# Performance work log

Measured on AMD Instinct MI355X. Metric: run time of the kernel, lower is better.

Reference implementation:

```python
import jax, jax.numpy as jnp
import numpy as np

EPS = 1e-5

def conv1x1(x, W, b):
    # x: (B,C,N,K), W: (O,C), b: (O,)
    return jnp.einsum('oc,bcnk->bonk', W, x) + b[None, :, None, None]

def group_norm(x, G, w, b):
    B, C, N, K = x.shape
    xg = x.reshape(B, G, C // G, N, K)
    mu = xg.mean(axis=(2, 3, 4), keepdims=True)
    var = xg.var(axis=(2, 3, 4), keepdims=True)
    xn = ((xg - mu) / jnp.sqrt(var + EPS)).reshape(B, C, N, K)
    return xn * w[None, :, None, None] + b[None, :, None, None]

def setup_inputs() -> dict:
    key = jax.random.key(0)
    ks = jax.random.split(key, 20)
    B, N, K = 4, 4096, 32
    C_in1, C_in2, C1, C2, C_out = 128, 128, 64, 64, 128
    Ccat = C1 + C2          # 128
    inter_C = min(Ccat, C_out)  # 128
    s = 0.05
    return {
        'feat': jax.random.normal(ks[0], (B, C_in1, N), jnp.float32),
        'grouped_feat': jax.random.normal(ks[1], (B, C_in2, N, K), jnp.float32),
        'grouped_feat_out': jax.random.normal(ks[2], (B, C_out, N, K), jnp.float32),
        'count': jax.random.randint(ks[3], (B, N), 0, K, jnp.int32),
        'W_feat': jax.random.normal(ks[4], (C1, C_in1), jnp.float32) * s,
        'b_feat': jax.random.normal(ks[5], (C1,), jnp.float32) * s,
        'W_grp': jax.random.normal(ks[6], (C2, C_in2), jnp.float32) * s,
        'b_grp': jax.random.normal(ks[7], (C2,), jnp.float32) * s,
        'gn1_w': jnp.ones((Ccat,), jnp.float32),
        'gn1_b': jnp.zeros((Ccat,), jnp.float32),
        'W_wc1': jax.random.normal(ks[8], (inter_C, Ccat), jnp.float32) * s,
        'b_wc1': jax.random.normal(ks[9], (inter_C,), jnp.float32) * s,
        'gn2_w': jnp.ones((inter_C,), jnp.float32),
        'gn2_b': jnp.zeros((inter_C,), jnp.float32),
        'W_wc2': jax.random.normal(ks[10], (C_out, inter_C), jnp.float32) * s,
        'b_wc2': jax.random.normal(ks[11], (C_out,), jnp.float32) * s,
        'W_fo': jax.random.normal(ks[12], (C_out, C_out), jnp.float32) * s,
        'b_fo': jax.random.normal(ks[13], (C_out,), jnp.float32) * s,
        'gn3_w': jnp.ones((C_out,), jnp.float32),
        'gn3_b': jnp.zeros((C_out,), jnp.float32),
    }

def reference(feat, grouped_feat, grouped_feat_out, count,
              W_feat, b_feat, W_grp, b_grp,
              gn1_w, gn1_b, W_wc1, b_wc1, gn2_w, gn2_b, W_wc2, b_wc2,
              W_fo, b_fo, gn3_w, gn3_b):
    K = grouped_feat.shape[-1]
    G = 32
    # feat_conv on feat.unsqueeze(-1), then expand along K
    feat1 = jnp.einsum('oc,bcn->bon', W_feat, feat) + b_feat[None, :, None]
    feat1 = jnp.broadcast_to(feat1[..., None], feat1.shape + (K,))
    g1 = conv1x1(grouped_feat, W_grp, b_grp)
    total = jnp.concatenate([feat1, g1], axis=1)  # (B, C1+C2, N, K)
    # weight_conv: ReLU -> GN -> conv -> ReLU -> GN -> conv
    x = jax.nn.relu(total)
    x = group_norm(x, G, gn1_w, gn1_b)
    x = conv1x1(x, W_wc1, b_wc1)
    x = jax.nn.relu(x)
    x = group_norm(x, G, gn2_w, gn2_b)
    scores = conv1x1(x, W_wc2, b_wc2)  # (B, C_out, N, K)
    # count-based mask over K, count clamped to >= 1
    cnt = jnp.clip(count, 1, None)
    mask = (jnp.arange(K)[None, None, :] < cnt[:, :, None]).astype(scores.dtype)  # (B,N,K)
    mask = mask[:, None, :, :]
    scores = scores * mask + (-1e9) * (1.0 - mask)
    weight = jax.nn.softmax(scores, axis=-1)
    # feat_out_conv: conv -> GN -> ReLU
    gfo = conv1x1(grouped_feat_out, W_fo, b_fo)
    gfo = jax.nn.relu(group_norm(gfo, G, gn3_w, gn3_b))
    return (gfo * weight).sum(axis=-1)  # (B, C_out, N)
```

## Files before the change

### kernel.cpp

```cpp
#include <hip/hip_runtime.h>


#define B_   4
#define N_   4096
#define KK_  32
#define NK_  131072
#define C_   128
#define EPSV 1e-5f

typedef _Float16 hf8 __attribute__((ext_vector_type(8)));
typedef _Float16 hf4 __attribute__((ext_vector_type(4)));
typedef float    f4  __attribute__((ext_vector_type(4)));

__global__ void prep_k(const float* __restrict__ Wgrp, const float* __restrict__ Wfo,
                       _Float16* __restrict__ Wgrp_h, _Float16* __restrict__ Wfo_h,
                       float* __restrict__ stats)
{
    int tid = blockIdx.x * 256 + threadIdx.x;
    if (tid < 64 * 128)  Wgrp_h[tid] = (_Float16)Wgrp[tid];
    if (tid < 128 * 128) Wfo_h[tid]  = (_Float16)Wfo[tid];
    if (tid < 768)       stats[tid]  = 0.0f;
}

__global__ void feat_k(const float* __restrict__ feat, const float* __restrict__ Wf,
                       const float* __restrict__ bfeat, float* __restrict__ f1r,
                       float* __restrict__ stats1)
{
    __shared__ float fs[128][64];
    __shared__ float gst[32];
    int tid = threadIdx.x, b = blockIdx.y, n0 = blockIdx.x * 64;
    if (tid < 32) gst[tid] = 0.0f;
    for (int i = tid; i < 128 * 64; i += 256) {
        int ci = i >> 6, n = i & 63;
        fs[ci][n] = feat[((size_t)b * 128 + ci) * N_ + n0 + n];
    }
    __syncthreads();
    int n = tid & 63, cb = (tid >> 6) * 16;
    float gs1[4] = {0,0,0,0}, gs2[4] = {0,0,0,0};
    for (int j = 0; j < 16; j++) {
        int c = cb + j;
        float a = bfeat[c];
        #pragma unroll 16
        for (int ci = 0; ci < 128; ci++) a += Wf[c * 128 + ci] * fs[ci][n];
        a = fmaxf(a, 0.0f);
        f1r[((size_t)b * 64 + c) * N_ + n0 + n] = a;
        gs1[j >> 2] += a; gs2[j >> 2] += a * a;
    }
    for (int g = 0; g < 4; g++) {
        atomicAdd(&gst[((cb >> 2) + g) * 2 + 0], gs1[g]);
        atomicAdd(&gst[((cb >> 2) + g) * 2 + 1], gs2[g]);
    }
    __syncthreads();
    if (tid < 32) atomicAdd(&stats1[b * 64 + tid], gst[tid]);
}

__global__ void fold_k(const float* __restrict__ stats, const float* __restrict__ gw,
                       const float* __restrict__ gb, const float* __restrict__ Wsrc,
                       const float* __restrict__ bsrc, _Float16* __restrict__ Wdst,
                       float* __restrict__ bdst, float* __restrict__ sdst,
                       float* __restrict__ tdst, int lowcnt)
{
    int b = blockIdx.x, tid = threadIdx.x;
    __shared__ float ss[128], st[128];
    if (tid < 128) {
        int c = tid, g = c >> 2;
        float d  = (lowcnt && g < 16) ? (4.0f * N_) : (4.0f * NK_);
        float S1 = stats[(b * 32 + g) * 2], S2 = stats[(b * 32 + g) * 2 + 1];
        float mu = S1 / d;
        float var = fmaxf(S2 / d - mu * mu, 0.0f);
        float s = gw[c] * rsqrtf(var + EPSV);
        float t = gb[c] - mu * s;
        ss[c] = s; st[c] = t;
        if (sdst) { sdst[b * 128 + c] = s; tdst[b * 128 + c] = t; }
    }
    __syncthreads();
    if (Wdst && tid < 128) {
        int co = tid;
        float a = bsrc[co];
        for (int c = 0; c < 128; c++) {
            float w = Wsrc[co * 128 + c];
            a += w * st[c];
            Wdst[((size_t)b * 128 + co) * 128 + c] = (_Float16)(w * ss[c]);
        }
        bdst[b * 128 + co] = a;
    }
}

__global__ void upass_k(const float* __restrict__ f1r, const _Float16* __restrict__ W1p,
                        const float* __restrict__ b1p, float* __restrict__ u)
{
    int b = blockIdx.y, n0 = blockIdx.x * 32, tid = threadIdx.x;
    __shared__ float fs[64][33];
    __shared__ _Float16 wl[128][68];
    for (int i = tid; i < 64 * 32; i += 256) {
        int c = i >> 5, n = i & 31;
        fs[c][n] = f1r[((size_t)b * 64 + c) * N_ + n0 + n];
    }
    for (int i = tid; i < 128 * 64; i += 256) {
        int co = i >> 6, c = i & 63;
        wl[co][c] = W1p[((size_t)b * 128 + co) * 128 + c];
    }
    __syncthreads();
    int co = tid & 127, nh = tid >> 7;
    float bb = b1p[b * 128 + co];
    for (int ps = 0; ps < 16; ps++) {
        int n = nh * 16 + ps;
        float a = bb;
        #pragma unroll 16
        for (int c = 0; c < 64; c++) a += (float)wl[co][c] * fs[c][n];
        u[((size_t)b * N_ + n0 + n) * C_ + co] = a;
    }
}

template<int CIN, int COUT, int TP, bool SRCF32, int EPI, bool HASU,
         int WRS, int WCOFF, int COOFF, bool WPB, bool BPB>
__global__ void __launch_bounds__(256, 2) gemm_k(
    const void* srcv, const _Float16* __restrict__ W, const float* __restrict__ bias,
    _Float16* out, float* __restrict__ stats, const float* __restrict__ u,
    const int* __restrict__ cnt)
{
    constexpr int KC  = CIN / 32;
    constexpr int WCO = (COUT == 128) ? 2 : 1;
    constexpr int WP  = 4 / WCO;
    constexpr int TILES = NK_ / TP;
    constexpr int NGR = TP / 32;

    __shared__ _Float16 xs[TP][CIN + 8];
    __shared__ float bstat[(EPI != 2) ? COUT * 2 : 1];
    __shared__ float uld[HASU ? NGR * COUT : 1];
    __shared__ int   cld[(EPI == 2) ? NGR : 1];

    const int tid  = threadIdx.x;
    const int lane = tid & 63;
    const int wave = tid >> 6;
    const int l15  = lane & 15;
    const int q    = lane >> 4;
    const int wm   = wave % WP;
    const int wn   = wave / WP;
    const int b    = blockIdx.y;

    hf8 bf[4][KC];
    const _Float16* Wb = W + (WPB ? (size_t)b * COUT * WRS : 0);
    #pragma unroll
    for (int nt = 0; nt < 4; nt++) {
        int co = wn * 64 + nt * 16 + l15;
        #pragma unroll
        for (int kc = 0; kc < KC; kc++)
            bf[nt][kc] = *(const hf8*)(Wb + (size_t)co * WRS + WCOFF + kc * 32 + q * 8);
    }
    float biasr[4];
    #pragma unroll
    for (int nt = 0; nt < 4; nt++) {
        int co = wn * 64 + nt * 16 + l15;
        biasr[nt] = bias ? bias[(BPB ? b * COUT : 0) + co] : 0.0f;
    }
    if (EPI != 2) for (int i = tid; i < COUT * 2; i += 256) bstat[i] = 0.0f;

    constexpr int TPG = TP / 4;
    constexpr int CQP = 256 / TPG;
    constexpr int PASSES = CIN / (4 * CQP);
    const int tp = tid % TPG;
    const int cq = tid / TPG;

    for (int t = blockIdx.x; t < TILES; t += gridDim.x) {
        const int pbase = t * TP;
        #pragma unroll
        for (int ps = 0; ps < PASSES; ps++) {
            int c0 = (ps * CQP + cq) * 4;
            _Float16 hv[4][4];
            if (SRCF32) {
                const float* s = (const float*)srcv;
                #pragma unroll
                for (int r = 0; r < 4; r++) {
                    f4 v = *(const f4*)(s + ((size_t)(b * CIN + c0 + r)) * NK_ + pbase + tp * 4);
                    #pragma unroll
                    for (int i = 0; i < 4; i++) hv[r][i] = (_Float16)v[i];
                }
            } else {
                const _Float16* s = (const _Float16*)srcv;
                #pragma unroll
                for (int r = 0; r < 4; r++) {
                    hf4 v = *(const hf4*)(s + ((size_t)(b * CIN + c0 + r)) * NK_ + pbase + tp * 4);
                    #pragma unroll
                    for (int i = 0; i < 4; i++) hv[r][i] = v[i];
                }
            }
            #pragma unroll
            for (int i = 0; i < 4; i++) {
                hf4 w = { hv[0][i], hv[1][i], hv[2][i], hv[3][i] };
                *(hf4*)&xs[tp * 4 + i][c0] = w;
            }
        }
        if (HASU)
            for (int i = tid; i < NGR * COUT; i += 256) {
                int ni = i / COUT, co = i % COUT;
                uld[ni * COUT + co] = u[((size_t)b * N_ + (pbase >> 5) + ni) * C_ + co];
            }
        if (EPI == 2 && tid < NGR) {
            int c = cnt[b * N_ + (pbase >> 5) + tid];
            cld[tid] = c < 1 ? 1 : c;
        }
        __syncthreads();

        f4 acc[4][4];
        #pragma unroll
        for (int mt = 0; mt < 4; mt++)
            #pragma unroll
            for (int nt = 0; nt < 4; nt++) {
                float v;
                if (HASU) v = uld[(wm * 2 + (mt >> 1)) * COUT + wn * 64 + nt * 16 + l15];
                else      v = biasr[nt];
                acc[mt][nt] = f4{v, v, v, v};
            }

        #pragma unroll
        for (int kc = 0; kc < KC; kc++) {
            hf8 af[4];
            #pragma unroll
            for (int mt = 0; mt < 4; mt++)
                af[mt] = *(const hf8*)&xs[wm * 64 + mt * 16 + l15][kc * 32 + q * 8];
            #pragma unroll
            for (int mt = 0; mt < 4; mt++)
                #pragma unroll
                for (int nt = 0; nt < 4; nt++)
                    acc[mt][nt] = __builtin_amdgcn_mfma_f32_16x16x32_f16(
                        af[mt], bf[nt][kc], acc[mt][nt], 0, 0, 0);
        }

        if constexpr (EPI != 2) {
            #pragma unroll
            for (int nt = 0; nt < 4; nt++) {
                int co = wn * 64 + nt * 16 + l15;
                float s1 = 0.0f, s2 = 0.0f;
                #pragma unroll
                for (int mt = 0; mt < 4; mt++) {
                    f4 a = acc[mt][nt];
                    #pragma unroll
                    for (int i = 0; i < 4; i++) {
                        if (EPI == 0) a[i] = fmaxf(a[i], 0.0f);
                        s1 += a[i]; s2 += a[i] * a[i];
                    }
                    hf4 hv = { (_Float16)a[0], (_Float16)a[1], (_Float16)a[2], (_Float16)a[3] };
                    *(hf4*)(out + ((size_t)(b * COUT + co)) * NK_ + pbase + wm * 64 + mt * 16 + q * 4) = hv;
                }
                s1 += __shfl_xor(s1, 16); s1 += __shfl_xor(s1, 32);
                s2 += __shfl_xor(s2, 16); s2 += __shfl_xor(s2, 32);
                if (q == 0) {
                    atomicAdd(&bstat[co * 2 + 0], s1);
                    atomicAdd(&bstat[co * 2 + 1], s2);
                }
            }
        } else {
            #pragma unroll
            for (int nt = 0; nt < 4; nt++) {
                float mx0 = -3e38f, mx1 = -3e38f;
                #pragma unroll
                for (int mt = 0; mt < 4; mt++) {
                    int cv = cld[wm * 2 + (mt >> 1)];
                    #pragma unroll
                    for (int r = 0; r < 4; r++) {
                        int k = (mt & 1) * 16 + q * 4 + r;
                        float v = acc[mt][nt][r];
                        if (k >= cv) v = -1e9f;
                        acc[mt][nt][r] = v;
                        if (mt < 2) mx0 = fmaxf(mx0, v); else mx1 = fmaxf(mx1, v);
                    }
                }
                mx0 = fmaxf(mx0, __shfl_xor(mx0, 16)); mx0 = fmaxf(mx0, __shfl_xor(mx0, 32));
                mx1 = fmaxf(mx1, __shfl_xor(mx1, 16)); mx1 = fmaxf(mx1, __shfl_xor(mx1, 32));
                float sm0 = 0.0f, sm1 = 0.0f;
                #pragma unroll
                for (int mt = 0; mt < 4; mt++) {
                    float m = (mt < 2) ? mx0 : mx1;
                    #pragma unroll
                    for (int r = 0; r < 4; r++) {
                        float e = __expf(acc[mt][nt][r] - m);
                        acc[mt][nt][r] = e;
                        if (mt < 2) sm0 += e; else sm1 += e;
                    }
                }
                sm0 += __shfl_xor(sm0, 16); sm0 += __shfl_xor(sm0, 32);
                sm1 += __shfl_xor(sm1, 16); sm1 += __shfl_xor(sm1, 32);
                float i0 = 1.0f / sm0, i1 = 1.0f / sm1;
                int co = wn * 64 + nt * 16 + l15;
                #pragma unroll
                for (int mt = 0; mt < 4; mt++) {
                    float inv = (mt < 2) ? i0 : i1;
                    hf4 hv = { (_Float16)(acc[mt][nt][0] * inv), (_Float16)(acc[mt][nt][1] * inv),
                               (_Float16)(acc[mt][nt][2] * inv), (_Float16)(acc[mt][nt][3] * inv) };
                    *(hf4*)(out + ((size_t)(b * COUT + co)) * NK_ + pbase + wm * 64 + mt * 16 + q * 4) = hv;
                }
            }
        }
        __syncthreads();
    }

    if (EPI != 2 && stats) {
        for (int i = tid; i < COUT * 2; i += 256) {
            int co = i >> 1, j = i & 1;
            int g = (co + COOFF) >> 2;
            atomicAdd(&stats[(b * 32 + g) * 2 + j], bstat[i]);
        }
    }
}

__global__ void final_k(const _Float16* __restrict__ y3, const _Float16* __restrict__ wgt,
                        const float* __restrict__ s3, const float* __restrict__ t3,
                        float* __restrict__ outp)
{
    int idx = blockIdx.x * 256 + threadIdx.x;
    int bc = idx >> 12;
    float sc = s3[bc], tc = t3[bc];
    const _Float16* yp = y3 + (size_t)idx * 32;
    const _Float16* wp = wgt + (size_t)idx * 32;
    float accv = 0.0f;
    #pragma unroll
    for (int i = 0; i < 4; i++) {
        hf8 yv = *(const hf8*)(yp + i * 8);
        hf8 wv = *(const hf8*)(wp + i * 8);
        #pragma unroll
        for (int j = 0; j < 8; j++) {
            float g = fmaxf(sc * (float)yv[j] + tc, 0.0f);
            accv += g * (float)wv[j];
        }
    }
    outp[idx] = accv;
}

extern "C" void kernel_launch(void* const* d_in, const int* in_sizes, int n_in,
                              void* d_out, int out_size, void* d_ws, size_t ws_size,
                              hipStream_t stream)
{
    (void)in_sizes; (void)n_in; (void)out_size; (void)ws_size;
    const float* feat   = (const float*)d_in[0];
    const float* gf     = (const float*)d_in[1];
    const float* gfo    = (const float*)d_in[2];
    const int*   count  = (const int*)d_in[3];
    const float* W_feat = (const float*)d_in[4];
    const float* b_feat = (const float*)d_in[5];
    const float* W_grp  = (const float*)d_in[6];
    const float* b_grp  = (const float*)d_in[7];
    const float* gn1w   = (const float*)d_in[8];
    const float* gn1b   = (const float*)d_in[9];
    const float* W_wc1  = (const float*)d_in[10];
    const float* b_wc1  = (const float*)d_in[11];
    const float* gn2w   = (const float*)d_in[12];
    const float* gn2b   = (const float*)d_in[13];
    const float* W_wc2  = (const float*)d_in[14];
    const float* b_wc2  = (const float*)d_in[15];
    const float* W_fo   = (const float*)d_in[16];
    const float* b_fo   = (const float*)d_in[17];
    const float* gn3w   = (const float*)d_in[18];
    const float* gn3b   = (const float*)d_in[19];
    float* out = (float*)d_out;

    char* ws = (char*)d_ws;
    size_t o = 0;
    auto alloc = [&](size_t bytes) { size_t r = o; o += (bytes + 255) & ~(size_t)255; return r; };
    _Float16* x1h    = (_Float16*)(ws + alloc((size_t)64 * B_ * NK_ * 2));
    _Float16* x2     = (_Float16*)(ws + alloc((size_t)128 * B_ * NK_ * 2));
    _Float16* y3     = (_Float16*)(ws + alloc((size_t)128 * B_ * NK_ * 2));
    float*    f1r    = (float*)(ws + alloc((size_t)B_ * 64 * N_ * 4));
    float*    u      = (float*)(ws + alloc((size_t)B_ * N_ * 128 * 4));
    float*    stats1 = (float*)(ws + alloc(256 * 4));
    float*    stats2 = (float*)(ws + alloc(256 * 4));
    float*    stats3 = (float*)(ws + alloc(256 * 4));
    _Float16* Wgrp_h = (_Float16*)(ws + alloc(64 * 128 * 2));
    _Float16* Wfo_h  = (_Float16*)(ws + alloc(128 * 128 * 2));
    _Float16* W1p    = (_Float16*)(ws + alloc((size_t)B_ * 128 * 128 * 2));
    float*    b1p    = (float*)(ws + alloc(B_ * 128 * 4));
    _Float16* W2p    = (_Float16*)(ws + alloc((size_t)B_ * 128 * 128 * 2));
    float*    b2p    = (float*)(ws + alloc(B_ * 128 * 4));
    float*    s3     = (float*)(ws + alloc(B_ * 128 * 4));
    float*    t3     = (float*)(ws + alloc(B_ * 128 * 4));
    _Float16* wgt    = x2;

    prep_k<<<64, 256, 0, stream>>>(W_grp, W_fo, Wgrp_h, Wfo_h, stats1);
    feat_k<<<dim3(64, B_), 256, 0, stream>>>(feat, W_feat, b_feat, f1r, stats1);
    gemm_k<128, 64, 256, true, 0, false, 128, 0, 64, false, false>
        <<<dim3(128, B_), 256, 0, stream>>>(gf, Wgrp_h, b_grp, x1h, stats1, nullptr, nullptr);
    fold_k<<<B_, 256, 0, stream>>>(stats1, gn1w, gn1b, W_wc1, b_wc1, W1p, b1p, nullptr, nullptr, 1);
    upass_k<<<dim3(128, B_), 256, 0, stream>>>(f1r, W1p, b1p, u);
    gemm_k<64, 128, 128, false, 0, true, 128, 64, 0, true, false>
        <<<dim3(256, B_), 256, 0, stream>>>(x1h, W1p, nullptr, x2, stats2, u, nullptr);
    gemm_k<128, 128, 128, true, 1, false, 128, 0, 0, false, false>
        <<<dim3(256, B_), 256, 0, stream>>>(gfo, Wfo_h, b_fo, y3, stats3, nullptr, nullptr);
    fold_k<<<B_, 256, 0, stream>>>(stats2, gn2w, gn2b, W_wc2, b_wc2, W2p, b2p, nullptr, nullptr, 0);
    fold_k<<<B_, 256, 0, stream>>>(stats3, gn3w, gn3b, nullptr, nullptr, nullptr, nullptr, s3, t3, 0);
    gemm_k<128, 128, 128, false, 2, false, 128, 0, 0, true, true>
        <<<dim3(256, B_), 256, 0, stream>>>(x2, W2p, b2p, wgt, nullptr, nullptr, count);
    final_k<<<(B_ * 128 * N_) / 256, 256, 0, stream>>>(y3, wgt, s3, t3, out);
}
```

Before: 1.226 ms.

## Prefetch next tile's inputs into registers to overlap with MFMA compute

Software-pipelines the persistent GEMM loop: the next tile's source activations, u-vectors and counts are loaded into registers while the current tile computes, and are written to LDS at the start of the following iteration. Full __syncthreads are replaced with raw s_barrier plus lgkmcnt waits, so the vmcnt drain is skipped and global loads can stay in flight across the barrier. This adds register pressure under launch_bounds(256,2), which may cause spills or lower occupancy, and the hand-placed barriers bring some risk of LDS races.

```diff
diff --git a/kernel.cpp b/kernel.cpp
--- a/kernel.cpp
+++ b/kernel.cpp
@@ -124,6 +124,12 @@
     constexpr int WP  = 4 / WCO;
     constexpr int TILES = NK_ / TP;
     constexpr int NGR = TP / 32;
+    constexpr int TPG = TP / 4;
+    constexpr int CQP = 256 / TPG;
+    constexpr int PASSES = CIN / (4 * CQP);
+    constexpr int PFP = (PASSES > 4) ? 4 : PASSES;
+    constexpr int RIP = PASSES - PFP;
+    constexpr int NU  = HASU ? (NGR * COUT / 256) : 1;
 
     __shared__ _Float16 xs[TP][CIN + 8];
     __shared__ float bstat[(EPI != 2) ? COUT * 2 : 1];
@@ -156,51 +162,108 @@
     }
     if (EPI != 2) for (int i = tid; i < COUT * 2; i += 256) bstat[i] = 0.0f;
 
-    constexpr int TPG = TP / 4;
-    constexpr int CQP = 256 / TPG;
-    constexpr int PASSES = CIN / (4 * CQP);
     const int tp = tid % TPG;
     const int cq = tid / TPG;
 
-    for (int t = blockIdx.x; t < TILES; t += gridDim.x) {
+    f4  Rf[SRCF32 ? PFP : 1][4];
+    hf4 Rh[SRCF32 ? 1 : PFP][4];
+    float ur[NU];
+    int   cr = 1;
+
+    auto prefetch = [&](int tt) {
+        const int pb = tt * TP;
+        #pragma unroll
+        for (int ps = 0; ps < PFP; ps++) {
+            const int c0 = (ps * CQP + cq) * 4;
+            #pragma unroll
+            for (int r = 0; r < 4; r++) {
+                const size_t off = ((size_t)(b * CIN + c0 + r)) * NK_ + pb + tp * 4;
+                if constexpr (SRCF32) Rf[ps][r] = *(const f4*)((const float*)srcv + off);
+                else                  Rh[ps][r] = *(const hf4*)((const _Float16*)srcv + off);
+            }
+        }
+        if constexpr (HASU) {
+            #pragma unroll
+            for (int j = 0; j < NU; j++) {
+                const int i = j * 256 + tid;
+                ur[j] = u[((size_t)b * N_ + (pb >> 5) + i / COUT) * C_ + (i % COUT)];
+            }
+        }
+        if constexpr (EPI == 2) {
+            if (tid < NGR) cr = cnt[b * N_ + (pb >> 5) + tid];
+        }
+    };
+
+    int t = blockIdx.x;
+    prefetch(t);
+
+    for (; t < TILES; t += (int)gridDim.x) {
         const int pbase = t * TP;
-        #pragma unroll
-        for (int ps = 0; ps < PASSES; ps++) {
-            int c0 = (ps * CQP + cq) * 4;
-            _Float16 hv[4][4];
-            if (SRCF32) {
-                const float* s = (const float*)srcv;
+
+        f4  R2f[(SRCF32 && RIP > 0) ? RIP : 1][4];
+        hf4 R2h[(!SRCF32 && RIP > 0) ? RIP : 1][4];
+        if constexpr (RIP > 0) {
+            #pragma unroll
+            for (int ps = 0; ps < RIP; ps++) {
+                const int c0 = ((PFP + ps) * CQP + cq) * 4;
                 #pragma unroll
                 for (int r = 0; r < 4; r++) {
-                    f4 v = *(const f4*)(s + ((size_t)(b * CIN + c0 + r)) * NK_ + pbase + tp * 4);
-                    #pragma unroll
-                    for (int i = 0; i < 4; i++) hv[r][i] = (_Float16)v[i];
-                }
-            } else {
-                const _Float16* s = (const _Float16*)srcv;
-                #pragma unroll
-                for (int r = 0; r < 4; r++) {
-                    hf4 v = *(const hf4*)(s + ((size_t)(b * CIN + c0 + r)) * NK_ + pbase + tp * 4);
-                    #pragma unroll
-                    for (int i = 0; i < 4; i++) hv[r][i] = v[i];
-                }
-            }
+                    const size_t off = ((size_t)(b * CIN + c0 + r)) * NK_ + pbase + tp * 4;
+                    if constexpr (SRCF32) R2f[ps][r] = *(const f4*)((const float*)srcv + off);
+                    else                  R2h[ps][r] = *(const hf4*)((const _Float16*)srcv + off);
+                }
+            }
+        }
+
+        asm volatile("" ::: "memory");
+        __builtin_amdgcn_s_barrier();
+        __builtin_amdgcn_sched_barrier(0);
+
+        #pragma unroll
+        for (int ps = 0; ps < PFP; ps++) {
+            const int c0 = (ps * CQP + cq) * 4;
             #pragma unroll
             for (int i = 0; i < 4; i++) {
-                hf4 w = { hv[0][i], hv[1][i], hv[2][i], hv[3][i] };
+                hf4 w;
+                if constexpr (SRCF32)
+                    w = hf4{ (_Float16)Rf[ps][0][i], (_Float16)Rf[ps][1][i],
+                             (_Float16)Rf[ps][2][i], (_Float16)Rf[ps][3][i] };
+                else
+                    w = hf4{ Rh[ps][0][i], Rh[ps][1][i], Rh[ps][2][i], Rh[ps][3][i] };
                 *(hf4*)&xs[tp * 4 + i][c0] = w;
             }
         }
-        if (HASU)
-            for (int i = tid; i < NGR * COUT; i += 256) {
-                int ni = i / COUT, co = i % COUT;
-                uld[ni * COUT + co] = u[((size_t)b * N_ + (pbase >> 5) + ni) * C_ + co];
-            }
-        if (EPI == 2 && tid < NGR) {
-            int c = cnt[b * N_ + (pbase >> 5) + tid];
-            cld[tid] = c < 1 ? 1 : c;
-        }
-        __syncthreads();
+        if constexpr (RIP > 0) {
+            #pragma unroll
+            for (int ps = 0; ps < RIP; ps++) {
+                const int c0 = ((PFP + ps) * CQP + cq) * 4;
+                #pragma unroll
+                for (int i = 0; i < 4; i++) {
+                    hf4 w;
+                    if constexpr (SRCF32)
+                        w = hf4{ (_Float16)R2f[ps][0][i], (_Float16)R2f[ps][1][i],
+                                 (_Float16)R2f[ps][2][i], (_Float16)R2f[ps][3][i] };
+                    else
+                        w = hf4{ R2h[ps][0][i], R2h[ps][1][i], R2h[ps][2][i], R2h[ps][3][i] };
+                    *(hf4*)&xs[tp * 4 + i][c0] = w;
+                }
+            }
+        }
+        if constexpr (HASU) {
+            #pragma unroll
+            for (int j = 0; j < NU; j++) uld[j * 256 + tid] = ur[j];
+        }
+        if constexpr (EPI == 2) {
+            if (tid < NGR) cld[tid] = cr < 1 ? 1 : cr;
+        }
+
+        const int tn = t + (int)gridDim.x;
+        if (tn < TILES) prefetch(tn);
+
+        asm volatile("s_waitcnt lgkmcnt(0)" ::: "memory");
+        __builtin_amdgcn_sched_barrier(0);
+        __builtin_amdgcn_s_barrier();
+        __builtin_amdgcn_sched_barrier(0);
 
         f4 acc[4][4];
         #pragma unroll
@@ -292,14 +355,19 @@
                 }
             }
         }
-        __syncthreads();
-    }
-
-    if (EPI != 2 && stats) {
-        for (int i = tid; i < COUT * 2; i += 256) {
-            int co = i >> 1, j = i & 1;
-            int g = (co + COOFF) >> 2;
-            atomicAdd(&stats[(b * 32 + g) * 2 + j], bstat[i]);
+    }
+
+    if constexpr (EPI != 2) {
+        asm volatile("s_waitcnt lgkmcnt(0)" ::: "memory");
+        __builtin_amdgcn_sched_barrier(0);
+        __builtin_amdgcn_s_barrier();
+        __builtin_amdgcn_sched_barrier(0);
+        if (stats) {
+            for (int i = tid; i < COUT * 2; i += 256) {
+                int co = i >> 1, j = i & 1;
+                int g = (co + COOFF) >> 2;
+                atomicAdd(&stats[(b * 32 + g) * 2 + j], bstat[i]);
+            }
         }
     }
 }
```

Result: slower. 1.302 ms (+6.2%).
